# Kernel tuning notes

Hardware: AMD Instinct MI355X
Metric: run time of the kernel (lower is better)

## Reference

```python
import jax, jax.numpy as jnp
import numpy as np

B, T, D, H = 64, 1024, 1024, 1024


def setup_inputs() -> dict:
    key = jax.random.key(0)
    k = jax.random.split(key, 5)
    s = 1.0 / np.sqrt(H)  # torch RNNCell init: U(-1/sqrt(H), 1/sqrt(H))
    return {
        "x": jax.random.normal(k[0], (B, T, D), jnp.float32),
        "W_ih": jax.random.uniform(k[1], (H, D), jnp.float32, -s, s),
        "W_hh": jax.random.uniform(k[2], (H, H), jnp.float32, -s, s),
        "b_ih": jax.random.uniform(k[3], (H,), jnp.float32, -s, s),
        "b_hh": jax.random.uniform(k[4], (H,), jnp.float32, -s, s),
    }


def reference(x, W_ih, W_hh, b_ih, b_hh):
    # DelayLineRNN2xOS with a tanh RNNCell:
    #   for i in range(T//2):
    #     h_eve = cell(x[:, 2i],   h_eve); states[:, 2i]   = h_eve
    #     h_odd = cell(x[:, 2i-1], h_odd); states[:, 2i-1] = h_odd   (note 2*0-1 == -1)
    Bn, Tn, _ = x.shape
    Hn = W_hh.shape[0]
    half = Tn // 2

    idx_eve = jnp.arange(half) * 2          # 0, 2, ..., T-2
    idx_odd = (idx_eve - 1) % Tn            # T-1, 1, 3, ..., T-3  (Python neg-index at i=0)

    # Precompute input projections for all timesteps (both biases folded in).
    gi = jnp.einsum('btd,hd->bth', x, W_ih) + b_ih + b_hh  # [B, T, H]
    ge = gi[:, idx_eve].transpose(1, 0, 2)                  # [half, B, H]
    go = gi[:, idx_odd].transpose(1, 0, 2)                  # [half, B, H]

    h0 = jnp.zeros((Bn, Hn), x.dtype)

    def step(carry, inp):
        he, ho = carry
        a, b = inp
        he = jnp.tanh(a + he @ W_hh.T)
        ho = jnp.tanh(b + ho @ W_hh.T)
        return (he, ho), (he, ho)

    (he_f, ho_f), (eve_s, odd_s) = jax.lax.scan(step, (h0, h0), (ge, go))

    # eve_s[i] -> slot 2i ; odd_s[i] -> slot (2i-1) mod T, i.e. sorted odd slots
    # [1, 3, ..., T-1] receive odd_s rolled left by one.
    odd_sorted = jnp.roll(odd_s, -1, axis=0)                # [half, B, H]
    states = jnp.stack([eve_s, odd_sorted], axis=1)         # [half, 2, B, H]
    states = states.reshape(Tn, Bn, Hn).transpose(1, 0, 2)  # [B, T, H]

    return states, he_f[None]  # (states, h_final[1, B, H])
```

## Files before the change

kernel.cpp:

```cpp
#include <hip/hip_runtime.h>

#define B_    64
#define T_    1024
#define H_    1024
#define HALF_ 512
#define NWG_SCAN 128
#define HBUF_HALF 131072

typedef short bf16x8 __attribute__((ext_vector_type(8)));
typedef short bf16x4 __attribute__((ext_vector_type(4)));
typedef _Float16 f16x8 __attribute__((ext_vector_type(8)));
typedef float f32x4  __attribute__((ext_vector_type(4)));
typedef unsigned int u32x4 __attribute__((ext_vector_type(4)));

__device__ __forceinline__ short f2bf(float f) {
    unsigned u = __builtin_bit_cast(unsigned, f);
    u += 0x7fffu + ((u >> 16) & 1u);
    return (short)(u >> 16);
}

__device__ __forceinline__ short f2h(float f) {
    return (short)__builtin_bit_cast(unsigned short, (_Float16)f);
}

__device__ __forceinline__ float tanh_fast(float x) {
    return 1.0f - 2.0f / (__expf(2.0f * x) + 1.0f);
}

#define BAR() do { \
    __builtin_amdgcn_sched_barrier(0); \
    asm volatile("s_waitcnt lgkmcnt(0)" ::: "memory"); \
    __builtin_amdgcn_sched_barrier(0); \
    __builtin_amdgcn_s_barrier(); \
    __builtin_amdgcn_sched_barrier(0); \
} while (0)

__global__ __launch_bounds__(256) void gi_gemm(
        const float* __restrict__ X, const float* __restrict__ Wih,
        const float* __restrict__ bih, const float* __restrict__ bhh,
        float* __restrict__ out) {
    __shared__ short As[128][40];
    __shared__ short Bs[128][40];
    const int bid = blockIdx.x;
    const int tn = bid & 7;
    const int tm = bid >> 3;
    const int tid = threadIdx.x;
    const int l  = tid & 63;
    const int w  = tid >> 6;
    const int wr = w >> 1, wc = w & 1;
    const int lc = l & 15,  lr = l >> 4;

    const float* Ab = X   + (size_t)tm * 128 * 1024;
    const float* Bb = Wih + (size_t)tn * 128 * 1024;
    const int srow = tid >> 3;
    const int sc4  = (tid & 7) * 4;

    f32x4 acc[4][4];
#pragma unroll
    for (int m = 0; m < 4; m++)
#pragma unroll
        for (int n = 0; n < 4; n++) acc[m][n] = (f32x4){0.f, 0.f, 0.f, 0.f};

    f32x4 ra[4], rb[4];
#pragma unroll
    for (int c = 0; c < 4; c++) {
        ra[c] = *reinterpret_cast<const f32x4*>(Ab + (size_t)(srow + 32*c) * 1024 + sc4);
        rb[c] = *reinterpret_cast<const f32x4*>(Bb + (size_t)(srow + 32*c) * 1024 + sc4);
    }

    for (int k0 = 0; k0 < 1024; k0 += 32) {
        __syncthreads();
#pragma unroll
        for (int c = 0; c < 4; c++) {
            bf16x4 va = { f2bf(ra[c].x), f2bf(ra[c].y), f2bf(ra[c].z), f2bf(ra[c].w) };
            bf16x4 vb = { f2bf(rb[c].x), f2bf(rb[c].y), f2bf(rb[c].z), f2bf(rb[c].w) };
            *reinterpret_cast<bf16x4*>(&As[srow + 32*c][sc4]) = va;
            *reinterpret_cast<bf16x4*>(&Bs[srow + 32*c][sc4]) = vb;
        }
        __syncthreads();
        if (k0 + 32 < 1024) {
            const float* Ak = Ab + k0 + 32;
            const float* Bk = Bb + k0 + 32;
#pragma unroll
            for (int c = 0; c < 4; c++) {
                ra[c] = *reinterpret_cast<const f32x4*>(Ak + (size_t)(srow + 32*c) * 1024 + sc4);
                rb[c] = *reinterpret_cast<const f32x4*>(Bk + (size_t)(srow + 32*c) * 1024 + sc4);
            }
        }
        bf16x8 af[4], bfr[4];
#pragma unroll
        for (int m = 0; m < 4; m++)
            af[m] = *reinterpret_cast<bf16x8*>(&As[wr*64 + m*16 + lc][lr*8]);
#pragma unroll
        for (int n = 0; n < 4; n++)
            bfr[n] = *reinterpret_cast<bf16x8*>(&Bs[wc*64 + n*16 + lc][lr*8]);
#pragma unroll
        for (int m = 0; m < 4; m++)
#pragma unroll
            for (int n = 0; n < 4; n++)
                acc[m][n] = __builtin_amdgcn_mfma_f32_16x16x32_bf16(af[m], bfr[n], acc[m][n], 0, 0, 0);
    }

#pragma unroll
    for (int n = 0; n < 4; n++) {
        const int col = tn*128 + wc*64 + n*16 + lc;
        const float bs = bih[col] + bhh[col];
#pragma unroll
        for (int m = 0; m < 4; m++) {
            const int row0 = tm*128 + wr*64 + m*16 + lr*4;
#pragma unroll
            for (int j = 0; j < 4; j++)
                out[(size_t)(row0 + j) * 1024 + col] = acc[m][n][j] + bs;
        }
    }
}

__global__ __launch_bounds__(256, 1) void rnn_scan(
        const float* __restrict__ Whh, float* __restrict__ out,
        short* __restrict__ hbuf) {
    __shared__ short hB[16 * 1024];
    __shared__ short htr[16 * 68];
    __shared__ float htrF[16 * 68];
    const int wg = blockIdx.x;
    const int p  = wg >> 6;
    const int g  = (wg >> 4) & 3;
    const int s  = wg & 15;
    const int tid = threadIdx.x;
    const int l  = tid & 63;
    const int w  = tid >> 6;
    const int lc = l & 15, lr = l >> 4;
    const int sb = tid >> 4;
    const int sg = tid & 15;

    bf16x8 breg[32];
    {
        const float* wrow = Whh + (size_t)(s*64 + w*16 + lc) * 1024;
#pragma unroll
        for (int kc = 0; kc < 32; kc++) {
            f32x4 v0 = *reinterpret_cast<const f32x4*>(wrow + kc*32 + lr*8);
            f32x4 v1 = *reinterpret_cast<const f32x4*>(wrow + kc*32 + lr*8 + 4);
            bf16x8 q = { f2h(v0.x), f2h(v0.y), f2h(v0.z), f2h(v0.w),
                         f2h(v1.x), f2h(v1.y), f2h(v1.z), f2h(v1.w) };
            breg[kc] = q;
        }
    }

    const unsigned hload_base = (unsigned)((p*64 + g*16 + sb) * 1024 + sg*8);
    const unsigned hstore_off = (unsigned)((p*64 + g*16 + sb) * 1024 + s*64 + sg*4);
    const int col = s*64 + w*16 + lc;

    for (int step = 0; step < HALF_; step++) {
        const int tt = (p == 0) ? (2*step) : (step == 0 ? T_-1 : 2*step - 1);
        const int epw = step % 3 + 1;
        const int epv = (step + 2) % 3 + 1;
        f32x4 acc = (f32x4){0.f, 0.f, 0.f, 0.f};
        float gi[4]; unsigned ob[4];

        if (step) {
            bf16x8 hl[8];
            const short* hc = hbuf + (size_t)((step+1) & 1) * HBUF_HALF + hload_base;
#pragma unroll
            for (int c = 0; c < 8; c++)
                asm volatile("global_load_dwordx4 %0, %1, off sc0 sc1"
                             : "=v"(hl[c]) : "v"(hc + c*128) : "memory");
#pragma unroll
            for (int j = 0; j < 4; j++) {
                ob[j] = (unsigned)(((g*16 + lr*4 + j) * T_ + tt) * H_ + col);
                gi[j] = out[ob[j]];
            }
            const unsigned pat = (unsigned)((epv & 1) | (((epv >> 1) & 1) << 16));
            unsigned pend = 0;
            asm volatile("s_waitcnt vmcnt(4)" ::: "memory");
            __builtin_amdgcn_sched_barrier(0);
#pragma unroll
            for (int c = 0; c < 8; c++) {
                u32x4 d = __builtin_bit_cast(u32x4, hl[c]);
                unsigned m = ((d[0] & 0x00010001u) ^ pat) | ((d[1] & 0x00010001u) ^ pat)
                           | ((d[2] & 0x00010001u) ^ pat) | ((d[3] & 0x00010001u) ^ pat);
                if (!__all(m == 0)) pend |= 1u << c;
            }
            while (pend) {
#pragma unroll
                for (int c = 0; c < 8; c++)
                    if (pend & (1u << c))
                        asm volatile("global_load_dwordx4 %0, %1, off sc0 sc1"
                                     : "=v"(hl[c]) : "v"(hc + c*128) : "memory");
                asm volatile("s_waitcnt vmcnt(0)" ::: "memory");
                __builtin_amdgcn_sched_barrier(0);
#pragma unroll
                for (int c = 0; c < 8; c++) {
                    if (pend & (1u << c)) {
                        u32x4 d = __builtin_bit_cast(u32x4, hl[c]);
                        unsigned m = ((d[0] & 0x00010001u) ^ pat) | ((d[1] & 0x00010001u) ^ pat)
                                   | ((d[2] & 0x00010001u) ^ pat) | ((d[3] & 0x00010001u) ^ pat);
                        if (__all(m == 0)) pend &= ~(1u << c);
                    }
                }
            }
#pragma unroll
            for (int c = 0; c < 8; c++) {
                bf16x4 lo = { hl[c][0], hl[c][1], hl[c][2], hl[c][3] };
                bf16x4 hi = { hl[c][4], hl[c][5], hl[c][6], hl[c][7] };
                const int g8 = (sg + c*16) * 2;
                *reinterpret_cast<bf16x4*>(&hB[sb*1024 + (((g8    ) ^ sb) << 2)]) = lo;
                *reinterpret_cast<bf16x4*>(&hB[sb*1024 + (((g8 + 1) ^ sb) << 2)]) = hi;
            }
            BAR();
            f32x4 a0 = (f32x4){0,0,0,0}, a1 = (f32x4){0,0,0,0};
            f32x4 a2 = (f32x4){0,0,0,0}, a3 = (f32x4){0,0,0,0};
#pragma unroll
            for (int kc = 0; kc < 32; kc += 4) {
#pragma unroll
                for (int q = 0; q < 4; q++) {
                    const int k8 = (kc + q) * 8 + lr * 2;
                    bf16x4 lo = *reinterpret_cast<const bf16x4*>(&hB[lc*1024 + (((k8    ) ^ lc) << 2)]);
                    bf16x4 hi = *reinterpret_cast<const bf16x4*>(&hB[lc*1024 + (((k8 + 1) ^ lc) << 2)]);
                    bf16x8 hf = { lo[0], lo[1], lo[2], lo[3], hi[0], hi[1], hi[2], hi[3] };
                    f32x4& aq = (q == 0) ? a0 : (q == 1) ? a1 : (q == 2) ? a2 : a3;
                    aq = __builtin_amdgcn_mfma_f32_16x16x32_f16(
                        __builtin_bit_cast(f16x8, hf),
                        __builtin_bit_cast(f16x8, breg[kc + q]), aq, 0, 0, 0);
                }
            }
            acc = (a0 + a1) + (a2 + a3);
        } else {
#pragma unroll
            for (int j = 0; j < 4; j++) {
                ob[j] = (unsigned)(((g*16 + lr*4 + j) * T_ + tt) * H_ + col);
                gi[j] = out[ob[j]];
            }
        }

        const unsigned short ebit = (unsigned short)((lc & 1) ? ((epw >> 1) & 1) : (epw & 1));
#pragma unroll
        for (int j = 0; j < 4; j++) {
            float hv = tanh_fast(acc[j] + gi[j]);
            unsigned short u = __builtin_bit_cast(unsigned short, (_Float16)hv);
            u = (unsigned short)((u & 0xFFFEu) | ebit);
            htr [(lr*4 + j)*68 + w*16 + lc] = (short)u;
            htrF[(lr*4 + j)*68 + w*16 + lc] = hv;
        }
        BAR();

        if (step < HALF_ - 1) {
            bf16x4 v = *reinterpret_cast<bf16x4*>(&htr[sb*68 + sg*4]);
            short* hn = hbuf + (size_t)(step & 1) * HBUF_HALF + hstore_off;
            asm volatile("global_store_dwordx2 %0, %1, off sc0 sc1"
                         :: "v"(hn), "v"(v) : "memory");
        }

        {
            f32x4 ov = *reinterpret_cast<f32x4*>(&htrF[sb*68 + sg*4]);
            float* op_ = out + (size_t)(((g*16 + sb) * T_ + tt) * H_ + s*64 + sg*4);
            asm volatile("global_store_dwordx4 %0, %1, off"
                         :: "v"(op_), "v"(ov) : "memory");
            if (p == 0 && step == HALF_ - 1) {
                float* fp_ = out + (size_t)B_*T_*H_ + (size_t)((g*16 + sb) * H_ + s*64 + sg*4);
                asm volatile("global_store_dwordx4 %0, %1, off"
                             :: "v"(fp_), "v"(ov) : "memory");
            }
        }
    }
}

extern "C" void kernel_launch(void* const* d_in, const int* in_sizes, int n_in,
                              void* d_out, int out_size, void* d_ws, size_t ws_size,
                              hipStream_t stream) {
    const float* X   = (const float*)d_in[0];
    const float* Wih = (const float*)d_in[1];
    const float* Whh = (const float*)d_in[2];
    const float* bih = (const float*)d_in[3];
    const float* bhh = (const float*)d_in[4];
    float* out = (float*)d_out;

    short* hbuf = (short*)d_ws;

    hipMemsetAsync(hbuf, 0, (size_t)2 * HBUF_HALF * 2, stream);
    gi_gemm<<<dim3(4096), dim3(256), 0, stream>>>(X, Wih, bih, bhh, out);
    rnn_scan<<<dim3(NWG_SCAN), dim3(256), 0, stream>>>(Whh, out, hbuf);
}
```

Baseline: 1.933 ms.

## Fuse input-projection GEMM into scan kernel with per-element ready flags

Merges the input-projection GEMM and the recurrent scan into one launch: the first 128 workgroups run the scan, and the remaining workgroups compute GEMM tiles in a time-ordered sequence (KORD). Each GEMM output sets its low mantissa bit as a ready flag. The scan spins until those flags appear, so it can start while later projections are still being computed. This hides the GEMM behind the serial scan, but the scan now polls with coherent loads and the forced low bit perturbs the stored values slightly. It also relies on the scan workgroups being resident together with the GEMM workgroups and on out being pre-zeroed or holding an even low bit.

```diff
diff --git a/kernel.cpp b/kernel.cpp
--- a/kernel.cpp
+++ b/kernel.cpp
@@ -5,6 +5,7 @@
 #define H_    1024
 #define HALF_ 512
 #define NWG_SCAN 128
+#define NWG_GEMM 4096
 #define HBUF_HALF 131072
 
 typedef short bf16x8 __attribute__((ext_vector_type(8)));
@@ -35,97 +36,107 @@
     __builtin_amdgcn_sched_barrier(0); \
 } while (0)
 
-__global__ __launch_bounds__(256) void gi_gemm(
+__global__ __launch_bounds__(256, 1) void fused_rnn(
         const float* __restrict__ X, const float* __restrict__ Wih,
         const float* __restrict__ bih, const float* __restrict__ bhh,
-        float* __restrict__ out) {
-    __shared__ short As[128][40];
-    __shared__ short Bs[128][40];
-    const int bid = blockIdx.x;
-    const int tn = bid & 7;
-    const int tm = bid >> 3;
-    const int tid = threadIdx.x;
-    const int l  = tid & 63;
-    const int w  = tid >> 6;
-    const int wr = w >> 1, wc = w & 1;
-    const int lc = l & 15,  lr = l >> 4;
-
-    const float* Ab = X   + (size_t)tm * 128 * 1024;
-    const float* Bb = Wih + (size_t)tn * 128 * 1024;
-    const int srow = tid >> 3;
-    const int sc4  = (tid & 7) * 4;
-
-    f32x4 acc[4][4];
-#pragma unroll
-    for (int m = 0; m < 4; m++)
-#pragma unroll
-        for (int n = 0; n < 4; n++) acc[m][n] = (f32x4){0.f, 0.f, 0.f, 0.f};
-
-    f32x4 ra[4], rb[4];
-#pragma unroll
-    for (int c = 0; c < 4; c++) {
-        ra[c] = *reinterpret_cast<const f32x4*>(Ab + (size_t)(srow + 32*c) * 1024 + sc4);
-        rb[c] = *reinterpret_cast<const f32x4*>(Bb + (size_t)(srow + 32*c) * 1024 + sc4);
-    }
-
-    for (int k0 = 0; k0 < 1024; k0 += 32) {
-        __syncthreads();
-#pragma unroll
-        for (int c = 0; c < 4; c++) {
-            bf16x4 va = { f2bf(ra[c].x), f2bf(ra[c].y), f2bf(ra[c].z), f2bf(ra[c].w) };
-            bf16x4 vb = { f2bf(rb[c].x), f2bf(rb[c].y), f2bf(rb[c].z), f2bf(rb[c].w) };
-            *reinterpret_cast<bf16x4*>(&As[srow + 32*c][sc4]) = va;
-            *reinterpret_cast<bf16x4*>(&Bs[srow + 32*c][sc4]) = vb;
-        }
-        __syncthreads();
-        if (k0 + 32 < 1024) {
-            const float* Ak = Ab + k0 + 32;
-            const float* Bk = Bb + k0 + 32;
-#pragma unroll
-            for (int c = 0; c < 4; c++) {
-                ra[c] = *reinterpret_cast<const f32x4*>(Ak + (size_t)(srow + 32*c) * 1024 + sc4);
-                rb[c] = *reinterpret_cast<const f32x4*>(Bk + (size_t)(srow + 32*c) * 1024 + sc4);
-            }
-        }
-        bf16x8 af[4], bfr[4];
-#pragma unroll
-        for (int m = 0; m < 4; m++)
-            af[m] = *reinterpret_cast<bf16x8*>(&As[wr*64 + m*16 + lc][lr*8]);
-#pragma unroll
-        for (int n = 0; n < 4; n++)
-            bfr[n] = *reinterpret_cast<bf16x8*>(&Bs[wc*64 + n*16 + lc][lr*8]);
-#pragma unroll
-        for (int m = 0; m < 4; m++)
-#pragma unroll
-            for (int n = 0; n < 4; n++)
-                acc[m][n] = __builtin_amdgcn_mfma_f32_16x16x32_bf16(af[m], bfr[n], acc[m][n], 0, 0, 0);
-    }
-
-#pragma unroll
-    for (int n = 0; n < 4; n++) {
-        const int col = tn*128 + wc*64 + n*16 + lc;
-        const float bs = bih[col] + bhh[col];
-#pragma unroll
-        for (int m = 0; m < 4; m++) {
-            const int row0 = tm*128 + wr*64 + m*16 + lr*4;
-#pragma unroll
-            for (int j = 0; j < 4; j++)
-                out[(size_t)(row0 + j) * 1024 + col] = acc[m][n][j] + bs;
-        }
-    }
-}
-
-__global__ __launch_bounds__(256, 1) void rnn_scan(
         const float* __restrict__ Whh, float* __restrict__ out,
         short* __restrict__ hbuf) {
-    __shared__ short hB[16 * 1024];
-    __shared__ short htr[16 * 68];
-    __shared__ float htrF[16 * 68];
+    __shared__ __align__(16) char smem[39296];
+    const int tid = threadIdx.x;
+
+    if (blockIdx.x >= NWG_SCAN) {
+        short (*As)[40] = reinterpret_cast<short(*)[40]>(smem);
+        short (*Bs)[40] = reinterpret_cast<short(*)[40]>(smem + 10240);
+        const int gb = blockIdx.x - NWG_SCAN;
+        const int tn = gb & 7;
+        const int u_ = gb >> 3;
+        const int b_ = u_ & 63;
+        const int kk = u_ >> 6;
+        const int KORD[8] = {0, 7, 1, 2, 3, 4, 5, 6};
+        const int tm = b_ * 8 + KORD[kk];
+        const int l  = tid & 63;
+        const int w  = tid >> 6;
+        const int wr = w >> 1, wc = w & 1;
+        const int lc = l & 15,  lr = l >> 4;
+
+        const float* Ab = X   + (size_t)tm * 128 * 1024;
+        const float* Bb = Wih + (size_t)tn * 128 * 1024;
+        const int srow = tid >> 3;
+        const int sc4  = (tid & 7) * 4;
+
+        f32x4 acc[4][4];
+#pragma unroll
+        for (int m = 0; m < 4; m++)
+#pragma unroll
+            for (int n = 0; n < 4; n++) acc[m][n] = (f32x4){0.f, 0.f, 0.f, 0.f};
+
+        f32x4 ra[4], rb[4];
+#pragma unroll
+        for (int c = 0; c < 4; c++) {
+            ra[c] = *reinterpret_cast<const f32x4*>(Ab + (size_t)(srow + 32*c) * 1024 + sc4);
+            rb[c] = *reinterpret_cast<const f32x4*>(Bb + (size_t)(srow + 32*c) * 1024 + sc4);
+        }
+
+        for (int k0 = 0; k0 < 1024; k0 += 32) {
+            __syncthreads();
+#pragma unroll
+            for (int c = 0; c < 4; c++) {
+                bf16x4 va = { f2bf(ra[c].x), f2bf(ra[c].y), f2bf(ra[c].z), f2bf(ra[c].w) };
+                bf16x4 vb = { f2bf(rb[c].x), f2bf(rb[c].y), f2bf(rb[c].z), f2bf(rb[c].w) };
+                *reinterpret_cast<bf16x4*>(&As[srow + 32*c][sc4]) = va;
+                *reinterpret_cast<bf16x4*>(&Bs[srow + 32*c][sc4]) = vb;
+            }
+            __syncthreads();
+            if (k0 + 32 < 1024) {
+                const float* Ak = Ab + k0 + 32;
+                const float* Bk = Bb + k0 + 32;
+#pragma unroll
+                for (int c = 0; c < 4; c++) {
+                    ra[c] = *reinterpret_cast<const f32x4*>(Ak + (size_t)(srow + 32*c) * 1024 + sc4);
+                    rb[c] = *reinterpret_cast<const f32x4*>(Bk + (size_t)(srow + 32*c) * 1024 + sc4);
+                }
+            }
+            bf16x8 af[4], bfr[4];
+#pragma unroll
+            for (int m = 0; m < 4; m++)
+                af[m] = *reinterpret_cast<bf16x8*>(&As[wr*64 + m*16 + lc][lr*8]);
+#pragma unroll
+            for (int n = 0; n < 4; n++)
+                bfr[n] = *reinterpret_cast<bf16x8*>(&Bs[wc*64 + n*16 + lc][lr*8]);
+#pragma unroll
+            for (int m = 0; m < 4; m++)
+#pragma unroll
+                for (int n = 0; n < 4; n++)
+                    acc[m][n] = __builtin_amdgcn_mfma_f32_16x16x32_bf16(af[m], bfr[n], acc[m][n], 0, 0, 0);
+        }
+
+#pragma unroll
+        for (int n = 0; n < 4; n++) {
+            const int col = tn*128 + wc*64 + n*16 + lc;
+            const float bs = bih[col] + bhh[col];
+#pragma unroll
+            for (int m = 0; m < 4; m++) {
+                const int row0 = tm*128 + wr*64 + m*16 + lr*4;
+#pragma unroll
+                for (int j = 0; j < 4; j++) {
+                    float v = acc[m][n][j] + bs;
+                    unsigned uv = __builtin_bit_cast(unsigned, v) | 1u;
+                    float* op_ = out + (size_t)(row0 + j) * 1024 + col;
+                    asm volatile("global_store_dword %0, %1, off sc0 sc1"
+                                 :: "v"(op_), "v"(uv) : "memory");
+                }
+            }
+        }
+        return;
+    }
+
+    short* hB   = reinterpret_cast<short*>(smem);
+    short* htr  = reinterpret_cast<short*>(smem + 32768);
+    float* htrF = reinterpret_cast<float*>(smem + 34944);
     const int wg = blockIdx.x;
     const int p  = wg >> 6;
     const int g  = (wg >> 4) & 3;
     const int s  = wg & 15;
-    const int tid = threadIdx.x;
     const int l  = tid & 63;
     const int w  = tid >> 6;
     const int lc = l & 15, lr = l >> 4;
@@ -154,7 +165,7 @@
         const int epw = step % 3 + 1;
         const int epv = (step + 2) % 3 + 1;
         f32x4 acc = (f32x4){0.f, 0.f, 0.f, 0.f};
-        float gi[4]; unsigned ob[4];
+        unsigned giu[4]; unsigned ob[4];
 
         if (step) {
             bf16x8 hl[8];
@@ -166,7 +177,9 @@
 #pragma unroll
             for (int j = 0; j < 4; j++) {
                 ob[j] = (unsigned)(((g*16 + lr*4 + j) * T_ + tt) * H_ + col);
-                gi[j] = out[ob[j]];
+                const float* ga = out + ob[j];
+                asm volatile("global_load_dword %0, %1, off sc0 sc1"
+                             : "=v"(giu[j]) : "v"(ga) : "memory");
             }
             const unsigned pat = (unsigned)((epv & 1) | (((epv >> 1) & 1) << 16));
             unsigned pend = 0;
@@ -227,14 +240,32 @@
 #pragma unroll
             for (int j = 0; j < 4; j++) {
                 ob[j] = (unsigned)(((g*16 + lr*4 + j) * T_ + tt) * H_ + col);
-                gi[j] = out[ob[j]];
-            }
+                const float* ga = out + ob[j];
+                asm volatile("global_load_dword %0, %1, off sc0 sc1"
+                             : "=v"(giu[j]) : "v"(ga) : "memory");
+            }
+        }
+
+        asm volatile("s_waitcnt vmcnt(0)" ::: "memory");
+        __builtin_amdgcn_sched_barrier(0);
+        while (true) {
+            unsigned okv = giu[0] & giu[1] & giu[2] & giu[3] & 1u;
+            if (__all(okv != 0)) break;
+#pragma unroll
+            for (int j = 0; j < 4; j++) {
+                const float* ga = out + ob[j];
+                asm volatile("global_load_dword %0, %1, off sc0 sc1"
+                             : "=v"(giu[j]) : "v"(ga) : "memory");
+            }
+            asm volatile("s_waitcnt vmcnt(0)" ::: "memory");
+            __builtin_amdgcn_sched_barrier(0);
         }
 
         const unsigned short ebit = (unsigned short)((lc & 1) ? ((epw >> 1) & 1) : (epw & 1));
 #pragma unroll
         for (int j = 0; j < 4; j++) {
-            float hv = tanh_fast(acc[j] + gi[j]);
+            float gv = __builtin_bit_cast(float, giu[j]);
+            float hv = tanh_fast(acc[j] + gv);
             unsigned short u = __builtin_bit_cast(unsigned short, (_Float16)hv);
             u = (unsigned short)((u & 0xFFFEu) | ebit);
             htr [(lr*4 + j)*68 + w*16 + lc] = (short)u;
@@ -276,6 +307,6 @@
     short* hbuf = (short*)d_ws;
 
     hipMemsetAsync(hbuf, 0, (size_t)2 * HBUF_HALF * 2, stream);
-    gi_gemm<<<dim3(4096), dim3(256), 0, stream>>>(X, Wih, bih, bhh, out);
-    rnn_scan<<<dim3(NWG_SCAN), dim3(256), 0, stream>>>(Whh, out, hbuf);
-}
+    fused_rnn<<<dim3(NWG_SCAN + NWG_GEMM), dim3(256), 0, stream>>>(
+        X, Wih, bih, bhh, Whh, out, hbuf);
+}
```

Result: slower. 2.101 ms (+8.7%).
